# Kernel optimization log

Measured on AMD Instinct MI355X. Metric: run time of the kernel, lower is better.

The kernel has to match this reference:

```python
import jax, jax.numpy as jnp
from jax import lax
import numpy as np

B, C, H, W = 32, 256, 56, 56
K = 3
EPS = 1e-5


def setup_inputs() -> dict:
    key = jax.random.key(0)
    k1, k2, k3, k4 = jax.random.split(key, 4)
    x = jax.random.normal(k1, (B, C, H, W), dtype=jnp.float32)
    # xavier_normal init for conv weight [C_out, C_in, K, K]
    fan_in = C * K * K
    fan_out = C * K * K
    std = float(np.sqrt(2.0 / (fan_in + fan_out)))
    w = jax.random.normal(k2, (C, C, K, K), dtype=jnp.float32) * std
    gamma = jnp.ones((C,), dtype=jnp.float32)
    beta = jnp.zeros((C,), dtype=jnp.float32)
    return {"x": x, "w": w, "gamma": gamma, "beta": beta}


def reference(x, w, gamma, beta):
    # --- Binarize (bi_act_method=0, bi_w_scale=1) ---
    bx = jnp.sign(x)                                   # activation sign
    wc = jnp.clip(w, -1.0, 1.0)                        # fp_weight.data.clamp_(-1,1)
    mean_val = jnp.mean(jnp.abs(wc))
    bw = jnp.sign(wc) * mean_val                       # sign(w) * mean(|w|)
    # --- float conv2d, stride 1, padding 1 ---
    out = lax.conv_general_dilated(
        bx, bw, window_strides=(1, 1), padding=[(1, 1), (1, 1)],
        dimension_numbers=("NCHW", "OIHW", "NCHW"))
    # --- identity shortcut (stride=1, C_in==C_out) ---
    out = out + x
    # --- BatchNorm2d (training-mode batch stats, affine) ---
    mean = jnp.mean(out, axis=(0, 2, 3), keepdims=True)
    var = jnp.var(out, axis=(0, 2, 3), keepdims=True)
    out = (out - mean) * lax.rsqrt(var + EPS)
    out = out * gamma[None, :, None, None] + beta[None, :, None, None]
    # --- ReLU ---
    return jax.nn.relu(out)
```

## Files before the change

kernel.cpp:

```cpp
#include <hip/hip_runtime.h>
#include <cstdint>

#define Bn   32
#define Cn   256
#define Hn   56
#define Wn   56
#define HWn  (Hn*Wn)
#define NTOT (Bn*Cn*HWn)
#define WELEMS (Cn*Cn*9)
#define EPSv 1e-5f

#define PR   58
#define PPB  (PR*PR)

#define F_WABS  0
#define F_SUM   64
#define F_SQ    320
#define STATS_BYTES 4096
#define CLS_OFF_BYTES 4096
#define WB_OFF_BYTES  16384
#define XB_OFF_BYTES  98304
#define XB_BYTES (Bn*PPB*8*4)

__global__ void pack_w_kernel(const float* __restrict__ w,
                              float* __restrict__ wsf,
                              uint32_t* __restrict__ wb) {
    int u = blockIdx.x * 256 + threadIdx.x;
    float sabs = 0.0f;
    {
        int co = u / 72;
        int r  = u % 72;
        int t  = r >> 3;
        int wd = r & 7;
        uint32_t bits = 0;
        const float* wp = w + (size_t)co * 2304 + (size_t)(wd * 32) * 9 + t;
        #pragma unroll
        for (int j = 0; j < 32; j++) {
            float wv = wp[(size_t)j * 9];
            sabs += fminf(fabsf(wv), 1.0f);
            bits |= (__float_as_uint(wv) >> 31) << j;
        }
        wb[u] = bits;
    }
    #pragma unroll
    for (int off = 32; off; off >>= 1) sabs += __shfl_down(sabs, off);
    __shared__ float sh[4];
    if ((threadIdx.x & 63) == 0) sh[threadIdx.x >> 6] = sabs;
    __syncthreads();
    if (threadIdx.x == 0)
        atomicAdd(&wsf[F_WABS], sh[0] + sh[1] + sh[2] + sh[3]);
}

__global__ void wtable_kernel(const uint32_t* __restrict__ wb,
                              int* __restrict__ clst) {
    int co = threadIdx.x;
    int wp[9];
    #pragma unroll
    for (int t = 0; t < 9; t++) {
        int s = 0;
        #pragma unroll
        for (int wd = 0; wd < 8; wd++) s += __popc(wb[(co * 9 + t) * 8 + wd]);
        wp[t] = 256 - 2 * s;
    }
    int T = wp[0] + wp[1] + wp[2];
    int Bm = wp[6] + wp[7] + wp[8];
    int L = wp[0] + wp[3] + wp[6];
    int R = wp[2] + wp[5] + wp[8];
    int* o = clst + co * 9;
    o[0] = 0;
    o[1] = L;
    o[2] = R;
    o[3] = T;
    o[4] = T + L - wp[0];
    o[5] = T + R - wp[2];
    o[6] = Bm;
    o[7] = Bm + L - wp[6];
    o[8] = Bm + R - wp[8];
}

__global__ void pack_x_kernel(const float* __restrict__ x,
                              uint32_t* __restrict__ xb) {
    int v = blockIdx.x * 256 + threadIdx.x;
    int b = v / HWn;
    int p = v - b * HWn;
    int y = p / Wn;
    int xq = p - y * Wn;
    const float* xp = x + (size_t)b * Cn * HWn + p;
    uint32_t r[8];
    #pragma unroll
    for (int wd = 0; wd < 8; wd++) {
        uint32_t bits = 0;
        #pragma unroll
        for (int j = 0; j < 32; j++) {
            bits |= (__float_as_uint(xp[(size_t)(wd * 32 + j) * HWn]) >> 31) << j;
        }
        r[wd] = bits;
    }
    size_t dst = (size_t)b * PPB + (size_t)(y + 1) * PR + (xq + 1);
    uint4* d = (uint4*)xb + dst * 2;
    d[0] = make_uint4(r[0], r[1], r[2], r[3]);
    d[1] = make_uint4(r[4], r[5], r[6], r[7]);
}

__global__ __launch_bounds__(256) void conv_kernel(
    const uint32_t* __restrict__ xb, const uint32_t* __restrict__ wb,
    const int* __restrict__ clst,
    const float* __restrict__ x, const float* __restrict__ wsf,
    float* __restrict__ out) {
    int v = blockIdx.x * 256 + threadIdx.x;
    int b = v / HWn;
    int p = v - b * HWn;
    int y = p / Wn;
    int xq = p - y * Wn;
    int co0 = blockIdx.y * 8;

    const float mean_val = wsf[F_WABS] * (1.0f / (float)WELEMS);

    const uint4* base = (const uint4*)xb + ((size_t)b * PPB + (size_t)y * PR + xq) * 2;

    int acc[8] = {0, 0, 0, 0, 0, 0, 0, 0};
    #pragma unroll
    for (int dh = 0; dh < 3; dh++) {
        uint32_t nw[24];
        const uint4* rp = base + dh * (PR * 2);
        #pragma unroll
        for (int q = 0; q < 6; q++) {
            uint4 t = rp[q];
            nw[q * 4 + 0] = t.x; nw[q * 4 + 1] = t.y;
            nw[q * 4 + 2] = t.z; nw[q * 4 + 3] = t.w;
        }
        #pragma unroll
        for (int dw = 0; dw < 3; dw++) {
            #pragma unroll
            for (int cs = 0; cs < 8; cs++) {
                const uint32_t* wp = wb + ((size_t)(co0 + cs) * 9 + (dh * 3 + dw)) * 8;
                int pc = acc[cs];
                #pragma unroll
                for (int wd = 0; wd < 8; wd++)
                    pc += __popc(nw[dw * 8 + wd] ^ wp[wd]);
                acc[cs] = pc;
            }
        }
    }

    int yp = (y == 0) ? 1 : ((y == 55) ? 2 : 0);
    int xp = (xq == 0) ? 1 : ((xq == 55) ? 2 : 0);
    int cls = yp * 3 + xp;

    #pragma unroll
    for (int cs = 0; cs < 8; cs++) {
        int corr = clst[(co0 + cs) * 9 + cls];
        size_t idx = ((size_t)b * Cn + (co0 + cs)) * HWn + p;
        float dot = (float)(2304 - 2 * acc[cs] - corr);
        out[idx] = fmaf(mean_val, dot, x[idx]);
    }
}

__global__ void stats_kernel(const float* __restrict__ out,
                             float* __restrict__ wsf) {
    int plane = blockIdx.x;
    const float4* p = (const float4*)(out + (size_t)plane * HWn);
    float s = 0.0f, q = 0.0f;
    for (int i = threadIdx.x; i < HWn / 4; i += 256) {
        float4 v = p[i];
        s += v.x + v.y + v.z + v.w;
        q += v.x * v.x + v.y * v.y + v.z * v.z + v.w * v.w;
    }
    #pragma unroll
    for (int off = 32; off; off >>= 1) {
        s += __shfl_down(s, off);
        q += __shfl_down(q, off);
    }
    __shared__ float ss[4], sq[4];
    if ((threadIdx.x & 63) == 0) { ss[threadIdx.x >> 6] = s; sq[threadIdx.x >> 6] = q; }
    __syncthreads();
    if (threadIdx.x == 0) {
        int c = plane & 255;
        atomicAdd(&wsf[F_SUM + c], ss[0] + ss[1] + ss[2] + ss[3]);
        atomicAdd(&wsf[F_SQ  + c], sq[0] + sq[1] + sq[2] + sq[3]);
    }
}

__global__ void epilogue_kernel(float* __restrict__ out,
                                const float* __restrict__ wsf,
                                const float* __restrict__ g,
                                const float* __restrict__ bt) {
    int plane = blockIdx.x;
    int c = plane & 255;
    const float n = (float)(Bn * HWn);
    float mean = wsf[F_SUM + c] / n;
    float var  = wsf[F_SQ + c] / n - mean * mean;
    float sc = g[c] * rsqrtf(var + EPSv);
    float sh = bt[c] - mean * sc;
    float4* o4 = (float4*)(out + (size_t)plane * HWn);
    for (int i = threadIdx.x; i < HWn / 4; i += 256) {
        float4 v = o4[i];
        v.x = fmaxf(fmaf(v.x, sc, sh), 0.0f);
        v.y = fmaxf(fmaf(v.y, sc, sh), 0.0f);
        v.z = fmaxf(fmaf(v.z, sc, sh), 0.0f);
        v.w = fmaxf(fmaf(v.w, sc, sh), 0.0f);
        o4[i] = v;
    }
}

extern "C" void kernel_launch(void* const* d_in, const int* in_sizes, int n_in,
                              void* d_out, int out_size, void* d_ws, size_t ws_size,
                              hipStream_t stream) {
    const float* x     = (const float*)d_in[0];
    const float* w     = (const float*)d_in[1];
    const float* gamma = (const float*)d_in[2];
    const float* beta  = (const float*)d_in[3];
    float* out = (float*)d_out;

    float*    wsf  = (float*)d_ws;
    int*      clst = (int*)((char*)d_ws + CLS_OFF_BYTES);
    uint32_t* wb   = (uint32_t*)((char*)d_ws + WB_OFF_BYTES);
    uint32_t* xb   = (uint32_t*)((char*)d_ws + XB_OFF_BYTES);

    hipMemsetAsync(d_ws, 0, STATS_BYTES, stream);
    hipMemsetAsync(xb, 0, XB_BYTES, stream);
    pack_w_kernel<<<dim3(72), dim3(256), 0, stream>>>(w, wsf, wb);
    wtable_kernel<<<dim3(1), dim3(256), 0, stream>>>(wb, clst);
    pack_x_kernel<<<dim3(392), dim3(256), 0, stream>>>(x, xb);
    conv_kernel<<<dim3(392, 32), dim3(256), 0, stream>>>(xb, wb, clst, x, wsf, out);
    stats_kernel<<<dim3(Bn * Cn), dim3(256), 0, stream>>>(out, wsf);
    epilogue_kernel<<<dim3(Bn * Cn), dim3(256), 0, stream>>>(out, wsf, gamma, beta);
}
```

Before: 354.5 us.

## Replace popcount binary conv with int8 MFMA implicit GEMM and fused BN stats

Encodes signed activations and weights as ±1 int8 in a padded layout with margins, so that a 3x3 convolution becomes an implicit GEMM over 9 taps using 32x32x32 int8 MFMA instructions. This replaces the XOR/popcount loop and its border-correction table. Batch-norm sum and sum-of-squares are now accumulated in the conv epilogue through an LDS transpose and shared atomics, which removes the separate stats pass and the big xb memset. The cost is a 256-byte-per-pixel int8 buffer, 8x larger than the bit-packed one, plus wasted MFMA work on padding pixels. Each block also reads A operands straight from global memory with no LDS staging.

```diff
diff --git a/kernel.cpp b/kernel.cpp
--- a/kernel.cpp
+++ b/kernel.cpp
@@ -1,47 +1,57 @@
 #include <hip/hip_runtime.h>
 #include <cstdint>
+#include <cstddef>
 
 #define Bn   32
 #define Cn   256
 #define Hn   56
 #define Wn   56
 #define HWn  (Hn*Wn)
-#define NTOT (Bn*Cn*HWn)
 #define WELEMS (Cn*Cn*9)
 #define EPSv 1e-5f
 
 #define PR   58
 #define PPB  (PR*PR)
-
-#define F_WABS  0
-#define F_SUM   64
-#define F_SQ    320
+#define NPP  (Bn*PPB)
+#define MARG 64
+
+#define F_WABS 0
+#define F_SUM  64
+#define F_SQ   320
 #define STATS_BYTES 4096
-#define CLS_OFF_BYTES 4096
-#define WB_OFF_BYTES  16384
-#define XB_OFF_BYTES  98304
-#define XB_BYTES (Bn*PPB*8*4)
+#define BPK_OFF 8192
+#define XI8_OFF 598016
+
+typedef int v4i  __attribute__((ext_vector_type(4)));
+typedef int v16i __attribute__((ext_vector_type(16)));
 
 __global__ void pack_w_kernel(const float* __restrict__ w,
                               float* __restrict__ wsf,
-                              uint32_t* __restrict__ wb) {
+                              int8_t* __restrict__ bpk) {
     int u = blockIdx.x * 256 + threadIdx.x;
+    int lane = u & 63;
+    int cob  = (u >> 6) & 7;
+    int cib  = (u >> 9) & 7;
+    int tap  = u >> 12;
+    int co  = cob * 32 + (lane & 31);
+    int ci0 = cib * 32 + (lane >> 5) * 16;
+
     float sabs = 0.0f;
-    {
-        int co = u / 72;
-        int r  = u % 72;
-        int t  = r >> 3;
-        int wd = r & 7;
-        uint32_t bits = 0;
-        const float* wp = w + (size_t)co * 2304 + (size_t)(wd * 32) * 9 + t;
-        #pragma unroll
-        for (int j = 0; j < 32; j++) {
-            float wv = wp[(size_t)j * 9];
+    uint32_t wrd[4];
+    #pragma unroll
+    for (int q = 0; q < 4; q++) {
+        uint32_t acc = 0;
+        #pragma unroll
+        for (int j = 0; j < 4; j++) {
+            float wv = w[((size_t)co * 256 + ci0 + q * 4 + j) * 9 + tap];
             sabs += fminf(fabsf(wv), 1.0f);
-            bits |= (__float_as_uint(wv) >> 31) << j;
-        }
-        wb[u] = bits;
-    }
+            uint32_t byte = (wv < 0.0f) ? 0xFFu : 0x01u;
+            acc |= byte << (8 * j);
+        }
+        wrd[q] = acc;
+    }
+    *(uint4*)(bpk + (size_t)u * 16) = make_uint4(wrd[0], wrd[1], wrd[2], wrd[3]);
+
     #pragma unroll
     for (int off = 32; off; off >>= 1) sabs += __shfl_down(sabs, off);
     __shared__ float sh[4];
@@ -51,140 +61,153 @@
         atomicAdd(&wsf[F_WABS], sh[0] + sh[1] + sh[2] + sh[3]);
 }
 
-__global__ void wtable_kernel(const uint32_t* __restrict__ wb,
-                              int* __restrict__ clst) {
-    int co = threadIdx.x;
-    int wp[9];
-    #pragma unroll
-    for (int t = 0; t < 9; t++) {
-        int s = 0;
-        #pragma unroll
-        for (int wd = 0; wd < 8; wd++) s += __popc(wb[(co * 9 + t) * 8 + wd]);
-        wp[t] = 256 - 2 * s;
-    }
-    int T = wp[0] + wp[1] + wp[2];
-    int Bm = wp[6] + wp[7] + wp[8];
-    int L = wp[0] + wp[3] + wp[6];
-    int R = wp[2] + wp[5] + wp[8];
-    int* o = clst + co * 9;
-    o[0] = 0;
-    o[1] = L;
-    o[2] = R;
-    o[3] = T;
-    o[4] = T + L - wp[0];
-    o[5] = T + R - wp[2];
-    o[6] = Bm;
-    o[7] = Bm + L - wp[6];
-    o[8] = Bm + R - wp[8];
-}
-
 __global__ void pack_x_kernel(const float* __restrict__ x,
-                              uint32_t* __restrict__ xb) {
-    int v = blockIdx.x * 256 + threadIdx.x;
-    int b = v / HWn;
-    int p = v - b * HWn;
-    int y = p / Wn;
-    int xq = p - y * Wn;
-    const float* xp = x + (size_t)b * Cn * HWn + p;
-    uint32_t r[8];
-    #pragma unroll
-    for (int wd = 0; wd < 8; wd++) {
-        uint32_t bits = 0;
-        #pragma unroll
-        for (int j = 0; j < 32; j++) {
-            bits |= (__float_as_uint(xp[(size_t)(wd * 32 + j) * HWn]) >> 31) << j;
-        }
-        r[wd] = bits;
-    }
-    size_t dst = (size_t)b * PPB + (size_t)(y + 1) * PR + (xq + 1);
-    uint4* d = (uint4*)xb + dst * 2;
-    d[0] = make_uint4(r[0], r[1], r[2], r[3]);
-    d[1] = make_uint4(r[4], r[5], r[6], r[7]);
+                              int8_t* __restrict__ xi8) {
+    int i = blockIdx.x * 256 + threadIdx.x;
+    long pp = (long)i - MARG;
+    int8_t* dst = xi8 + (size_t)i * 256;
+
+    bool interior = false;
+    int b = 0, p = 0;
+    if (pp >= 0 && pp < NPP) {
+        b = (int)(pp / PPB);
+        int r = (int)(pp - (long)b * PPB);
+        int row = r / PR;
+        int col = r - row * PR;
+        if (row >= 1 && row <= 56 && col >= 1 && col <= 56) {
+            interior = true;
+            p = (row - 1) * Wn + (col - 1);
+        }
+    }
+
+    if (interior) {
+        const float* xp = x + (size_t)b * Cn * HWn + p;
+        #pragma unroll
+        for (int q = 0; q < 16; q++) {
+            uint32_t wrd[4];
+            #pragma unroll
+            for (int k = 0; k < 4; k++) {
+                uint32_t acc = 0;
+                #pragma unroll
+                for (int j = 0; j < 4; j++) {
+                    float v = xp[(size_t)(q * 16 + k * 4 + j) * HWn];
+                    uint32_t byte = (v < 0.0f) ? 0xFFu : 0x01u;
+                    acc |= byte << (8 * j);
+                }
+                wrd[k] = acc;
+            }
+            *(uint4*)(dst + q * 16) = make_uint4(wrd[0], wrd[1], wrd[2], wrd[3]);
+        }
+    } else {
+        uint4 z = make_uint4(0, 0, 0, 0);
+        #pragma unroll
+        for (int q = 0; q < 16; q++) *(uint4*)(dst + q * 16) = z;
+    }
 }
 
 __global__ __launch_bounds__(256) void conv_kernel(
-    const uint32_t* __restrict__ xb, const uint32_t* __restrict__ wb,
-    const int* __restrict__ clst,
-    const float* __restrict__ x, const float* __restrict__ wsf,
+    const int8_t* __restrict__ xi8p,
+    const int8_t* __restrict__ bpk,
+    const float* __restrict__ x, float* __restrict__ wsf,
     float* __restrict__ out) {
-    int v = blockIdx.x * 256 + threadIdx.x;
-    int b = v / HWn;
-    int p = v - b * HWn;
-    int y = p / Wn;
-    int xq = p - y * Wn;
-    int co0 = blockIdx.y * 8;
-
-    const float mean_val = wsf[F_WABS] * (1.0f / (float)WELEMS);
-
-    const uint4* base = (const uint4*)xb + ((size_t)b * PPB + (size_t)y * PR + xq) * 2;
-
-    int acc[8] = {0, 0, 0, 0, 0, 0, 0, 0};
-    #pragma unroll
-    for (int dh = 0; dh < 3; dh++) {
-        uint32_t nw[24];
-        const uint4* rp = base + dh * (PR * 2);
-        #pragma unroll
-        for (int q = 0; q < 6; q++) {
-            uint4 t = rp[q];
-            nw[q * 4 + 0] = t.x; nw[q * 4 + 1] = t.y;
-            nw[q * 4 + 2] = t.z; nw[q * 4 + 3] = t.w;
-        }
-        #pragma unroll
-        for (int dw = 0; dw < 3; dw++) {
+    const int tid = threadIdx.x;
+    const int w = tid >> 6, l = tid & 63;
+    const int wrow = w & 1, wcol = w >> 1;
+
+    __shared__ int   lds[64 * 129];
+    __shared__ float ssum[128], ssq[128];
+    if (tid < 128) { ssum[tid] = 0.0f; ssq[tid] = 0.0f; }
+
+    const long pp0 = (long)blockIdx.x * 128 + wrow * 64;
+    const int8_t* Abase0 = xi8p + (pp0 + (l & 31)) * 256 + (l >> 5) * 16;
+    const int8_t* Bbase = bpk + ((size_t)(blockIdx.y * 4 + wcol * 2) * 64 + l) * 16;
+
+    v16i acc[2][2] = {};
+
+    for (int tap = 0; tap < 9; tap++) {
+        int toff = (tap / 3) * 58 + (tap % 3) - 59;
+        const int8_t* At0 = Abase0 + (long)toff * 256;
+        const int8_t* At1 = At0 + 32 * 256;
+        const int8_t* Bt  = Bbase + (size_t)tap * 65536;
+        #pragma unroll
+        for (int cib = 0; cib < 8; cib++) {
+            v4i a0 = *(const v4i*)(At0 + cib * 32);
+            v4i a1 = *(const v4i*)(At1 + cib * 32);
+            v4i b0 = *(const v4i*)(Bt + cib * 8192);
+            v4i b1 = *(const v4i*)(Bt + cib * 8192 + 1024);
+            acc[0][0] = __builtin_amdgcn_mfma_i32_32x32x32_i8(a0, b0, acc[0][0], 0, 0, 0);
+            acc[0][1] = __builtin_amdgcn_mfma_i32_32x32x32_i8(a0, b1, acc[0][1], 0, 0, 0);
+            acc[1][0] = __builtin_amdgcn_mfma_i32_32x32x32_i8(a1, b0, acc[1][0], 0, 0, 0);
+            acc[1][1] = __builtin_amdgcn_mfma_i32_32x32x32_i8(a1, b1, acc[1][1], 0, 0, 0);
+        }
+    }
+
+    const float mv = wsf[F_WABS] * (1.0f / (float)WELEMS);
+
+    bool   val[2];
+    size_t pix[2];
+    #pragma unroll
+    for (int ph = 0; ph < 2; ph++) {
+        long pp = (long)blockIdx.x * 128 + ph * 64 + l;
+        int b = (int)(pp / PPB);
+        int r = (int)(pp - (long)b * PPB);
+        int row = r / PR;
+        int col = r - row * PR;
+        val[ph] = (row >= 1 && row <= 56 && col >= 1 && col <= 56);
+        int p = (row - 1) * Wn + (col - 1);
+        pix[ph] = (size_t)b * (Cn * HWn) + p;
+    }
+
+    #pragma unroll
+    for (int ph = 0; ph < 2; ph++) {
+        __syncthreads();
+        if (wrow == ph) {
             #pragma unroll
-            for (int cs = 0; cs < 8; cs++) {
-                const uint32_t* wp = wb + ((size_t)(co0 + cs) * 9 + (dh * 3 + dw)) * 8;
-                int pc = acc[cs];
+            for (int s = 0; s < 2; s++)
                 #pragma unroll
-                for (int wd = 0; wd < 8; wd++)
-                    pc += __popc(nw[dw * 8 + wd] ^ wp[wd]);
-                acc[cs] = pc;
-            }
-        }
-    }
-
-    int yp = (y == 0) ? 1 : ((y == 55) ? 2 : 0);
-    int xp = (xq == 0) ? 1 : ((xq == 55) ? 2 : 0);
-    int cls = yp * 3 + xp;
-
-    #pragma unroll
-    for (int cs = 0; cs < 8; cs++) {
-        int corr = clst[(co0 + cs) * 9 + cls];
-        size_t idx = ((size_t)b * Cn + (co0 + cs)) * HWn + p;
-        float dot = (float)(2304 - 2 * acc[cs] - corr);
-        out[idx] = fmaf(mean_val, dot, x[idx]);
-    }
-}
-
-__global__ void stats_kernel(const float* __restrict__ out,
-                             float* __restrict__ wsf) {
-    int plane = blockIdx.x;
-    const float4* p = (const float4*)(out + (size_t)plane * HWn);
-    float s = 0.0f, q = 0.0f;
-    for (int i = threadIdx.x; i < HWn / 4; i += 256) {
-        float4 v = p[i];
-        s += v.x + v.y + v.z + v.w;
-        q += v.x * v.x + v.y * v.y + v.z * v.z + v.w * v.w;
-    }
-    #pragma unroll
-    for (int off = 32; off; off >>= 1) {
-        s += __shfl_down(s, off);
-        q += __shfl_down(q, off);
-    }
-    __shared__ float ss[4], sq[4];
-    if ((threadIdx.x & 63) == 0) { ss[threadIdx.x >> 6] = s; sq[threadIdx.x >> 6] = q; }
+                for (int t = 0; t < 2; t++)
+                    #pragma unroll
+                    for (int r = 0; r < 16; r++) {
+                        int mrow = s * 32 + 4 * (l >> 5) + 8 * (r >> 2) + (r & 3);
+                        int ncol = wcol * 64 + t * 32 + (l & 31);
+                        lds[mrow * 129 + ncol] = acc[s][t][r];
+                    }
+        }
+        __syncthreads();
+        for (int i = 0; i < 32; i++) {
+            int colco = i * 4 + w;
+            int co = blockIdx.y * 128 + colco;
+            float pre = 0.0f;
+            if (val[ph]) {
+                int dot = lds[l * 129 + colco];
+                size_t idx = pix[ph] + (size_t)co * HWn;
+                pre = fmaf(mv, (float)dot, x[idx]);
+                out[idx] = pre;
+            }
+            float s1 = pre, s2 = pre * pre;
+            #pragma unroll
+            for (int off = 32; off; off >>= 1) {
+                s1 += __shfl_down(s1, off);
+                s2 += __shfl_down(s2, off);
+            }
+            if (l == 0) {
+                atomicAdd(&ssum[colco], s1);
+                atomicAdd(&ssq[colco], s2);
+            }
+        }
+    }
     __syncthreads();
-    if (threadIdx.x == 0) {
-        int c = plane & 255;
-        atomicAdd(&wsf[F_SUM + c], ss[0] + ss[1] + ss[2] + ss[3]);
-        atomicAdd(&wsf[F_SQ  + c], sq[0] + sq[1] + sq[2] + sq[3]);
-    }
-}
-
-__global__ void epilogue_kernel(float* __restrict__ out,
-                                const float* __restrict__ wsf,
-                                const float* __restrict__ g,
-                                const float* __restrict__ bt) {
+    if (tid < 128) {
+        int co = blockIdx.y * 128 + tid;
+        atomicAdd(&wsf[F_SUM + co], ssum[tid]);
+        atomicAdd(&wsf[F_SQ  + co], ssq[tid]);
+    }
+}
+
+__global__ void bnrelu_kernel(float* __restrict__ out,
+                              const float* __restrict__ wsf,
+                              const float* __restrict__ g,
+                              const float* __restrict__ bt) {
     int plane = blockIdx.x;
     int c = plane & 255;
     const float n = (float)(Bn * HWn);
@@ -212,17 +235,14 @@
     const float* beta  = (const float*)d_in[3];
     float* out = (float*)d_out;
 
-    float*    wsf  = (float*)d_ws;
-    int*      clst = (int*)((char*)d_ws + CLS_OFF_BYTES);
-    uint32_t* wb   = (uint32_t*)((char*)d_ws + WB_OFF_BYTES);
-    uint32_t* xb   = (uint32_t*)((char*)d_ws + XB_OFF_BYTES);
+    float*  wsf = (float*)d_ws;
+    int8_t* bpk = (int8_t*)d_ws + BPK_OFF;
+    int8_t* xi8 = (int8_t*)d_ws + XI8_OFF;
+    const int8_t* xi8p = xi8 + (size_t)MARG * 256;
 
     hipMemsetAsync(d_ws, 0, STATS_BYTES, stream);
-    hipMemsetAsync(xb, 0, XB_BYTES, stream);
-    pack_w_kernel<<<dim3(72), dim3(256), 0, stream>>>(w, wsf, wb);
-    wtable_kernel<<<dim3(1), dim3(256), 0, stream>>>(wb, clst);
-    pack_x_kernel<<<dim3(392), dim3(256), 0, stream>>>(x, xb);
-    conv_kernel<<<dim3(392, 32), dim3(256), 0, stream>>>(xb, wb, clst, x, wsf, out);
-    stats_kernel<<<dim3(Bn * Cn), dim3(256), 0, stream>>>(out, wsf);
-    epilogue_kernel<<<dim3(Bn * Cn), dim3(256), 0, stream>>>(out, wsf, gamma, beta);
-}
+    pack_w_kernel<<<dim3(144), dim3(256), 0, stream>>>(w, wsf, bpk);
+    pack_x_kernel<<<dim3(421), dim3(256), 0, stream>>>(x, xi8);
+    conv_kernel<<<dim3(841, 2), dim3(256), 0, stream>>>(xi8p, bpk, x, wsf, out);
+    bnrelu_kernel<<<dim3(Bn * Cn), dim3(256), 0, stream>>>(out, wsf, gamma, beta);
+}
```

After: 522.1 us. 1.47x slower.
